# Optimization experiments

Hardware: AMD Instinct MI355X
Metric: run time of the kernel (lower is better)

Reference implementation:

```python
import jax, jax.numpy as jnp
import numpy as np

NUM_AGENTS = 256
STATE_DIM = 12 * NUM_AGENTS
CONTROL_DIM = 4 * NUM_AGENTS
MASS = 0.5
HIDDEN = 100
BATCH = 8192


def lambertw(x):
    # Principal branch for x >= 0 via Halley iterations (jit/vjp friendly).
    w = jnp.log1p(x)
    for _ in range(30):
        ew = jnp.exp(w)
        f = w * ew - x
        denom = ew * (w + 1.0) - (w + 2.0) * f / (2.0 * (w + 1.0))
        w = w - f / denom
    return w


def setup_inputs() -> dict:
    key = jax.random.key(0)
    ks = jax.random.split(key, 8)
    scale1 = 1.0 / np.sqrt(STATE_DIM + 1)
    scale2 = 1.0 / np.sqrt(HIDDEN)
    return {
        "z": jax.random.normal(ks[0], (BATCH, STATE_DIM), dtype=jnp.float32),
        "t": jax.random.uniform(ks[1], (BATCH, 1), dtype=jnp.float32),
        "W1": jax.random.normal(ks[2], (STATE_DIM + 1, HIDDEN), dtype=jnp.float32) * scale1,
        "b1": jnp.zeros((HIDDEN,), dtype=jnp.float32),
        "W2": jax.random.normal(ks[3], (HIDDEN, HIDDEN), dtype=jnp.float32) * scale2,
        "b2": jnp.zeros((HIDDEN,), dtype=jnp.float32),
        "W3": jax.random.normal(ks[4], (HIDDEN, STATE_DIM), dtype=jnp.float32) * scale2,
        "b3": jnp.zeros((STATE_DIM,), dtype=jnp.float32),
    }


def reference(z, t, W1, b1, W2, b2, W3, b3):
    # p_net: MLP on (t, z) producing cost parameters p (B, STATE_DIM)
    x = jnp.concatenate([t, z], axis=-1)
    h = jnp.tanh(x @ W1 + b1)
    h = jnp.tanh(h @ W2 + b2)
    p = h @ W3 + b3

    B = p.shape[0]
    pr = p.reshape(B, NUM_AGENTS, 12)
    # Linear cost vector c over controls: agent components (x,y,z adjoints)/m, psi, theta, phi.
    c = jnp.stack(
        [(pr[..., 6] + pr[..., 7] + pr[..., 8]) / MASS, pr[..., 9], pr[..., 10], pr[..., 11]],
        axis=-1,
    ).reshape(B, CONTROL_DIM)

    # Closed-form solution of min_u c^T u + exp(alpha * ||u||^2), alpha = 0.5/N:
    # u* = -k c with 2*alpha*k*exp(alpha*k^2*s) = 1, s = ||c||^2
    # => k = sqrt(W(s/(2*alpha)) / (2*alpha*s))
    alpha = 0.5 / NUM_AGENTS
    s = jnp.sum(c * c, axis=-1)  # (B,)
    w = lambertw(s / (2.0 * alpha))
    safe_s = jnp.where(s > 0, s, 1.0)
    k = jnp.sqrt(w / (2.0 * alpha * safe_s))
    k = jnp.where(s > 0, k, 0.0)
    ustar = -k[:, None] * c  # (B, CONTROL_DIM)
    return ustar
```

## Files before the change

### kernel.cpp

```cpp
#include <hip/hip_runtime.h>

#define DEV __device__ __forceinline__

typedef __bf16 bf16x8 __attribute__((ext_vector_type(8)));
typedef float f32x4 __attribute__((ext_vector_type(4)));
typedef short s16x8 __attribute__((ext_vector_type(8)));
typedef unsigned short u16x4 __attribute__((ext_vector_type(4)));
typedef unsigned short u16x8 __attribute__((ext_vector_type(8)));

constexpr int B_ = 8192;
constexpr int S_ = 3072;
constexpr int H_ = 100;
constexpr int NP_ = 128;
constexpr int C_ = 1024;
constexpr int KS_ = 64;
constexpr int NSPLIT_ = 4;
constexpr int KSP_ = S_ / NSPLIT_;
constexpr int NIT_ = KSP_ / KS_;

constexpr size_t OFF_W1b = 0;
constexpr size_t OFF_W2b = OFF_W1b + (size_t)NP_ * S_ * 2;
constexpr size_t OFF_W3c = OFF_W2b + (size_t)NP_ * NP_ * 2;
constexpr size_t OFF_b3c = OFF_W3c + (size_t)C_ * NP_ * 2;
constexpr size_t OFF_part = OFF_b3c + (size_t)C_ * 4;

DEV unsigned short f2bf(float f) {
  union { float f; unsigned u; } x; x.f = f;
  return (unsigned short)((x.u + 0x7FFFu + ((x.u >> 16) & 1u)) >> 16);
}

DEV float lambertw0(float x) {
  float w = log1pf(x);
#pragma unroll
  for (int i = 0; i < 10; ++i) {
    float ew = expf(w);
    float f = fmaf(w, ew, -x);
    float wp1 = w + 1.0f;
    float den = ew * wp1 - (w + 2.0f) * f / (2.0f * wp1);
    w = w - f / den;
  }
  return w;
}

DEV void gload16(const void* g, void* l) {
  __builtin_amdgcn_global_load_lds((const __attribute__((address_space(1))) unsigned int*)g,
                                   (__attribute__((address_space(3))) unsigned int*)l, 16, 0, 0);
}

__global__ void k0_prep(const float* __restrict__ W1, const float* __restrict__ W2,
                        const float* __restrict__ W3, const float* __restrict__ b3,
                        unsigned char* __restrict__ ws) {
  int idx = blockIdx.x * 256 + threadIdx.x;
  constexpr int R1 = NP_ * S_;
  constexpr int R2 = R1 + NP_ * NP_;
  constexpr int R3 = R2 + C_ * NP_;
  constexpr int R4 = R3 + C_;
  if (idx < R1) {
    int n = idx / S_, k = idx - n * S_;
    float v = (n < H_) ? W1[(size_t)(k + 1) * H_ + n] : 0.0f;
    ((unsigned short*)(ws + OFF_W1b))[idx] = f2bf(v);
  } else if (idx < R2) {
    int j = idx - R1;
    int n = j >> 7, k = j & 127;
    float v = (n < H_ && k < H_) ? W2[(size_t)k * H_ + n] : 0.0f;
    ((unsigned short*)(ws + OFF_W2b))[j] = f2bf(v);
  } else if (idx < R3) {
    int j = idx - R2;
    int n = j >> 7, k = j & 127;
    float v = 0.0f;
    if (k < H_) {
      int a = n >> 2, cmp = n & 3;
      const float* row = W3 + (size_t)k * S_ + a * 12;
      v = (cmp == 0) ? 2.0f * (row[6] + row[7] + row[8]) : row[8 + cmp];
    }
    ((unsigned short*)(ws + OFF_W3c))[j] = f2bf(v);
  } else if (idx < R4) {
    int n = idx - R3;
    int a = n >> 2, cmp = n & 3;
    const float* row = b3 + a * 12;
    float v = (cmp == 0) ? 2.0f * (row[6] + row[7] + row[8]) : row[8 + cmp];
    ((float*)(ws + OFF_b3c))[n] = v;
  }
}

__global__ __launch_bounds__(256, 4) void k1_gemm1(
    const float* __restrict__ z, const unsigned char* __restrict__ wsr,
    float* __restrict__ part) {
  __shared__ __align__(16) unsigned char lds[40 * 1024];
  unsigned char* ldsA = lds;
  unsigned char* ldsB = lds + 8192;

  const int tid = threadIdx.x;
  const int lane = tid & 63;
  const int w = tid >> 6;
  const int m = w & 1;
  const int q = w >> 1;
  const int bid = blockIdx.x;
  const int rt = bid >> 2;
  const int h = bid & 3;
  const int rowbase = rt * 32;
  const int k0 = h * KSP_;

  const unsigned short* W1b = (const unsigned short*)(wsr + OFF_W1b);

  const int arow0 = tid >> 4;
  const int acolf = (tid & 15) * 4;
  const float* zp = z + (size_t)(rowbase + arow0) * S_ + k0 + acolf;
  const int aswz = ((arow0 & 7) << 4);
  const int abyte0 = arow0 * 128 + (tid & 15) * 8;
  const int abyte1 = (arow0 + 16) * 128 + (tid & 15) * 8;

  const int w4 = w * 4;
  const unsigned short* bsrc = W1b + (size_t)(w4 * 8 + (lane >> 3)) * S_ + k0
                               + (((lane & 7) ^ (lane >> 3)) * 8);

  const int r0 = m * 16 + (lane & 15);
  const int kb0 = (lane >> 4) * 16;

  f32x4 acc[4];
#pragma unroll
  for (int e = 0; e < 4; ++e) acc[e] = f32x4{0.f, 0.f, 0.f, 0.f};

#define GLOAD_B(bufoff, kof) do {                                            \
    _Pragma("unroll")                                                        \
    for (int s = 0; s < 4; ++s)                                              \
      gload16(bsrc + (size_t)s * 8 * S_ + (kof),                             \
              ldsB + (bufoff) + (w4 + s) * 1024);                            \
  } while (0)

#define STAGE_A(dst, Z0, Z1) do {                                            \
    u16x4 a0; a0[0] = f2bf((Z0).x); a0[1] = f2bf((Z0).y);                    \
    a0[2] = f2bf((Z0).z); a0[3] = f2bf((Z0).w);                              \
    u16x4 a1; a1[0] = f2bf((Z1).x); a1[1] = f2bf((Z1).y);                    \
    a1[2] = f2bf((Z1).z); a1[3] = f2bf((Z1).w);                              \
    *(u16x4*)((dst) + (abyte0 ^ aswz)) = a0;                                 \
    *(u16x4*)((dst) + (abyte1 ^ aswz)) = a1;                                 \
  } while (0)

#define COMPUTE(Ac, Bc) do {                                                 \
    bf16x8 a0 = *(const bf16x8*)((Ac) + ((r0 * 128 + 0 + kb0) ^ ((r0 & 7) << 4)));   \
    bf16x8 a1 = *(const bf16x8*)((Ac) + ((r0 * 128 + 64 + kb0) ^ ((r0 & 7) << 4)));  \
    _Pragma("unroll")                                                        \
    for (int e = 0; e < 4; ++e) {                                            \
      int n = q * 64 + e * 16 + (lane & 15);                                 \
      bf16x8 bb0 = *(const bf16x8*)((Bc) + ((n * 128 + 0 + kb0) ^ ((n & 7) << 4)));  \
      bf16x8 bb1 = *(const bf16x8*)((Bc) + ((n * 128 + 64 + kb0) ^ ((n & 7) << 4))); \
      acc[e] = __builtin_amdgcn_mfma_f32_16x16x32_bf16(a0, bb0, acc[e], 0, 0, 0);    \
      acc[e] = __builtin_amdgcn_mfma_f32_16x16x32_bf16(a1, bb1, acc[e], 0, 0, 0);    \
    }                                                                        \
  } while (0)

  GLOAD_B(0, 0);
  {
    float4 z0 = *(const float4*)(zp);
    float4 z1 = *(const float4*)(zp + (size_t)16 * S_);
    STAGE_A(ldsA, z0, z1);
  }
  __syncthreads();

  for (int it = 0; it < NIT_; ++it) {
    const int cur = it & 1;
    const bool more = (it + 1 < NIT_);
    float4 z0, z1;
    if (more) {
      GLOAD_B((cur ^ 1) * 16384, (size_t)(it + 1) * KS_);
      z0 = *(const float4*)(zp + (it + 1) * KS_);
      z1 = *(const float4*)(zp + (size_t)16 * S_ + (it + 1) * KS_);
    }
    COMPUTE(ldsA + cur * 4096, ldsB + cur * 16384);
    if (more) STAGE_A(ldsA + (cur ^ 1) * 4096, z0, z1);
    __syncthreads();
  }
#undef GLOAD_B
#undef STAGE_A
#undef COMPUTE

  float* pout = part + (size_t)h * B_ * NP_;
#pragma unroll
  for (int e = 0; e < 4; ++e) {
    int col = q * 64 + e * 16 + (lane & 15);
#pragma unroll
    for (int i = 0; i < 4; ++i) {
      int r = m * 16 + ((lane >> 4) << 2) + i;
      pout[(size_t)(rowbase + r) * NP_ + col] = acc[e][i];
    }
  }
}

__global__ __launch_bounds__(512, 2) void k2_fused(
    const float* __restrict__ part, const float* __restrict__ t,
    const float* __restrict__ W1, const float* __restrict__ b1,
    const float* __restrict__ b2, const unsigned char* __restrict__ wsr,
    float* __restrict__ uo) {
  __shared__ __align__(16) unsigned char ldsA[8192];
  __shared__ __align__(16) unsigned char ldsB[2][32768];
  __shared__ float s_part[32][4];
  __shared__ float k_lds[32];

  const int tid = threadIdx.x;
  const int lane = tid & 63;
  const int w = tid >> 6;
  const int m = w & 1;
  const int q = w >> 1;
  const int rowbase = blockIdx.x * 32;

  const unsigned short* W2b = (const unsigned short*)(wsr + OFF_W2b);
  const unsigned short* W3cb = (const unsigned short*)(wsr + OFF_W3c);
  const float* b3c = (const float*)(wsr + OFF_b3c);

  {
    const int row = tid >> 4;
    const int col0 = (tid & 15) * 8;
    const float* p0 = part + (size_t)(rowbase + row) * NP_ + col0;
    f32x4 v[2];
#pragma unroll
    for (int p = 0; p < 2; ++p) {
      v[p] = *(const f32x4*)(p0 + p * 4);
#pragma unroll
      for (int hh = 1; hh < NSPLIT_; ++hh) {
        f32x4 u2 = *(const f32x4*)(p0 + (size_t)hh * B_ * NP_ + p * 4);
        v[p][0] += u2[0]; v[p][1] += u2[1]; v[p][2] += u2[2]; v[p][3] += u2[3];
      }
    }
    const float tv = t[rowbase + row];
    u16x8 o;
#pragma unroll
    for (int j = 0; j < 8; ++j) {
      int col = col0 + j;
      float b1c = (col < H_) ? b1[col] : 0.0f;
      float w1t = (col < H_) ? W1[col] : 0.0f;
      float pre = v[j >> 2][j & 3] + b1c + tv * w1t;
      o[j] = f2bf(tanhf(pre));
    }
    *(u16x8*)(ldsA + ((row * 256 + col0 * 2) ^ ((row & 7) << 4))) = o;
  }
#pragma unroll
  for (int s = 0; s < 4; ++s) {
    int p = s * 512 + tid;
    int n = p >> 4, k16 = p & 15;
    s16x8 v2 = *(const s16x8*)(W2b + n * 128 + k16 * 8);
    *(s16x8*)(ldsB[1] + ((n * 256 + k16 * 16) ^ ((n & 7) << 4))) = v2;
    s16x8 v3 = *(const s16x8*)(W3cb + (size_t)n * NP_ + k16 * 8);
    *(s16x8*)(ldsB[0] + ((n * 256 + k16 * 16) ^ ((n & 7) << 4))) = v3;
  }
  if (tid < 128) s_part[tid >> 2][tid & 3] = 0.0f;
  __syncthreads();

  const int r0 = m * 16 + (lane & 15);
  const int kb0 = (lane >> 4) * 16;

  f32x4 acc2[2];
  acc2[0] = f32x4{0.f, 0.f, 0.f, 0.f};
  acc2[1] = f32x4{0.f, 0.f, 0.f, 0.f};
#pragma unroll
  for (int ks = 0; ks < 4; ++ks) {
    bf16x8 a = *(const bf16x8*)(ldsA + ((r0 * 256 + ks * 64 + kb0) ^ ((r0 & 7) << 4)));
#pragma unroll
    for (int e = 0; e < 2; ++e) {
      int n = (q * 2 + e) * 16 + (lane & 15);
      bf16x8 b = *(const bf16x8*)(ldsB[1] + ((n * 256 + ks * 64 + kb0) ^ ((n & 7) << 4)));
      acc2[e] = __builtin_amdgcn_mfma_f32_16x16x32_bf16(a, b, acc2[e], 0, 0, 0);
    }
  }
  __syncthreads();
#pragma unroll
  for (int e = 0; e < 2; ++e) {
    int col = (q * 2 + e) * 16 + (lane & 15);
    float b2c = (col < H_) ? b2[col] : 0.0f;
#pragma unroll
    for (int i = 0; i < 4; ++i) {
      int r = m * 16 + ((lane >> 4) << 2) + i;
      float hh = tanhf(acc2[e][i] + b2c);
      *(unsigned short*)(ldsA + ((r * 256 + col * 2) ^ ((r & 7) << 4))) = f2bf(hh);
    }
  }
  __syncthreads();

  bf16x8 af[4];
#pragma unroll
  for (int ks = 0; ks < 4; ++ks)
    af[ks] = *(const bf16x8*)(ldsA + ((r0 * 256 + ks * 64 + kb0) ^ ((r0 & 7) << 4)));

  f32x4 fr[16];
#pragma unroll
  for (int i = 0; i < 16; ++i) fr[i] = f32x4{0.f, 0.f, 0.f, 0.f};

#pragma unroll 8
  for (int ch = 0; ch < 8; ++ch) {
    const int cur = ch & 1;
    const bool more = ch < 7;
    s16x8 st0, st1, st2, st3;
    if (more) {
      int base = (ch + 1) * 128;
      { int p = tid;            int n = p >> 4, k16 = p & 15; st0 = *(const s16x8*)(W3cb + (size_t)(base + n) * NP_ + k16 * 8); }
      { int p = 512 + tid;      int n = p >> 4, k16 = p & 15; st1 = *(const s16x8*)(W3cb + (size_t)(base + n) * NP_ + k16 * 8); }
      { int p = 1024 + tid;     int n = p >> 4, k16 = p & 15; st2 = *(const s16x8*)(W3cb + (size_t)(base + n) * NP_ + k16 * 8); }
      { int p = 1536 + tid;     int n = p >> 4, k16 = p & 15; st3 = *(const s16x8*)(W3cb + (size_t)(base + n) * NP_ + k16 * 8); }
    }
#pragma unroll
    for (int e = 0; e < 2; ++e) {
      int nloc = (q + 4 * e) * 16 + (lane & 15);
#pragma unroll
      for (int ks = 0; ks < 4; ++ks) {
        bf16x8 b = *(const bf16x8*)(ldsB[cur] + ((nloc * 256 + ks * 64 + kb0) ^ ((nloc & 7) << 4)));
        fr[ch * 2 + e] = __builtin_amdgcn_mfma_f32_16x16x32_bf16(af[ks], b, fr[ch * 2 + e], 0, 0, 0);
      }
    }
    if (more) {
      unsigned char* Bn = ldsB[cur ^ 1];
      { int p = tid;        int n = p >> 4, k16 = p & 15; *(s16x8*)(Bn + ((n * 256 + k16 * 16) ^ ((n & 7) << 4))) = st0; }
      { int p = 512 + tid;  int n = p >> 4, k16 = p & 15; *(s16x8*)(Bn + ((n * 256 + k16 * 16) ^ ((n & 7) << 4))) = st1; }
      { int p = 1024 + tid; int n = p >> 4, k16 = p & 15; *(s16x8*)(Bn + ((n * 256 + k16 * 16) ^ ((n & 7) << 4))) = st2; }
      { int p = 1536 + tid; int n = p >> 4, k16 = p & 15; *(s16x8*)(Bn + ((n * 256 + k16 * 16) ^ ((n & 7) << 4))) = st3; }
    }
    __syncthreads();
  }

#pragma unroll
  for (int fi = 0; fi < 16; ++fi) {
    int ch = fi >> 1, e = fi & 1;
    int col = (ch * 8 + q + 4 * e) * 16 + (lane & 15);
    float bc = b3c[col];
    fr[fi][0] += bc; fr[fi][1] += bc; fr[fi][2] += bc; fr[fi][3] += bc;
  }
#pragma unroll
  for (int i = 0; i < 4; ++i) {
    float v = 0.f;
#pragma unroll
    for (int fi = 0; fi < 16; ++fi) v += fr[fi][i] * fr[fi][i];
    v += __shfl_xor(v, 1);
    v += __shfl_xor(v, 2);
    v += __shfl_xor(v, 4);
    v += __shfl_xor(v, 8);
    if ((lane & 15) == 0) s_part[m * 16 + ((lane >> 4) << 2) + i][q] = v;
  }
  __syncthreads();
  if (tid < 32) {
    float s = s_part[tid][0] + s_part[tid][1] + s_part[tid][2] + s_part[tid][3];
    float kk = 0.0f;
    if (s > 0.0f) {
      float wv = lambertw0(s * 256.0f);
      kk = sqrtf(wv * 256.0f / s);
    }
    k_lds[tid] = kk;
  }
  __syncthreads();
#pragma unroll
  for (int fi = 0; fi < 16; ++fi) {
    int ch = fi >> 1, e = fi & 1;
    int col = (ch * 8 + q + 4 * e) * 16 + (lane & 15);
#pragma unroll
    for (int i = 0; i < 4; ++i) {
      int r = m * 16 + ((lane >> 4) << 2) + i;
      uo[(size_t)(rowbase + r) * C_ + col] = -k_lds[r] * fr[fi][i];
    }
  }
}

extern "C" void kernel_launch(void* const* d_in, const int* in_sizes, int n_in,
                              void* d_out, int out_size, void* d_ws, size_t ws_size,
                              hipStream_t stream) {
  const float* z  = (const float*)d_in[0];
  const float* t  = (const float*)d_in[1];
  const float* W1 = (const float*)d_in[2];
  const float* b1 = (const float*)d_in[3];
  const float* W2 = (const float*)d_in[4];
  const float* b2 = (const float*)d_in[5];
  const float* W3 = (const float*)d_in[6];
  const float* b3 = (const float*)d_in[7];
  float* out = (float*)d_out;
  unsigned char* ws = (unsigned char*)d_ws;
  float* part = (float*)(ws + OFF_part);

  constexpr int PREP_ELEMS = NP_ * S_ + NP_ * NP_ + C_ * NP_ + C_;
  k0_prep<<<(PREP_ELEMS + 255) / 256, 256, 0, stream>>>(W1, W2, W3, b3, ws);
  k1_gemm1<<<B_ / 32 * NSPLIT_, 256, 0, stream>>>(z, ws, part);
  k2_fused<<<B_ / 32, 512, 0, stream>>>(part, t, W1, b1, b2, ws, out);
}
```

Baseline: 51.52 us.

## Shrink gemm1 row tile to 16 and drop LDS double buffering for occupancy

The first GEMM kernel now processes 16 rows per block instead of 32, so twice as many blocks launch, and each wave computes two 16-column tiles instead of four. The LDS double buffer is replaced by a single buffer with two barriers per iteration, cutting LDS use from 40KB to about 18KB, and launch bounds are raised to 8 blocks per CU. The aim is more occupancy and parallelism to hide memory latency. In exchange, every W1 tile is reloaded twice as often, and global loads no longer overlap with compute inside a block.

```diff
diff --git a/kernel.cpp b/kernel.cpp
--- a/kernel.cpp
+++ b/kernel.cpp
@@ -17,6 +17,7 @@
 constexpr int NSPLIT_ = 4;
 constexpr int KSP_ = S_ / NSPLIT_;
 constexpr int NIT_ = KSP_ / KS_;
+constexpr int MT_ = 16;
 
 constexpr size_t OFF_W1b = 0;
 constexpr size_t OFF_W2b = OFF_W1b + (size_t)NP_ * S_ * 2;
@@ -83,93 +84,81 @@
   }
 }
 
-__global__ __launch_bounds__(256, 4) void k1_gemm1(
+__global__ __launch_bounds__(256, 8) void k1_gemm1(
     const float* __restrict__ z, const unsigned char* __restrict__ wsr,
     float* __restrict__ part) {
-  __shared__ __align__(16) unsigned char lds[40 * 1024];
-  unsigned char* ldsA = lds;
-  unsigned char* ldsB = lds + 8192;
+  __shared__ __align__(16) unsigned char ldsA[2048];
+  __shared__ __align__(16) unsigned char ldsB[16384];
 
   const int tid = threadIdx.x;
   const int lane = tid & 63;
   const int w = tid >> 6;
-  const int m = w & 1;
-  const int q = w >> 1;
   const int bid = blockIdx.x;
   const int rt = bid >> 2;
   const int h = bid & 3;
-  const int rowbase = rt * 32;
+  const int rowbase = rt * MT_;
   const int k0 = h * KSP_;
 
   const unsigned short* W1b = (const unsigned short*)(wsr + OFF_W1b);
 
-  const int arow0 = tid >> 4;
-  const int acolf = (tid & 15) * 4;
-  const float* zp = z + (size_t)(rowbase + arow0) * S_ + k0 + acolf;
-  const int aswz = ((arow0 & 7) << 4);
-  const int abyte0 = arow0 * 128 + (tid & 15) * 8;
-  const int abyte1 = (arow0 + 16) * 128 + (tid & 15) * 8;
+  const int arow = tid >> 4;
+  const float* zp = z + (size_t)(rowbase + arow) * S_ + k0 + (tid & 15) * 4;
+  const int aswz = ((arow & 7) << 4);
+  const int abyte = arow * 128 + (tid & 15) * 8;
 
   const int w4 = w * 4;
   const unsigned short* bsrc = W1b + (size_t)(w4 * 8 + (lane >> 3)) * S_ + k0
                                + (((lane & 7) ^ (lane >> 3)) * 8);
 
-  const int r0 = m * 16 + (lane & 15);
+  const int r0 = lane & 15;
   const int kb0 = (lane >> 4) * 16;
 
-  f32x4 acc[4];
-#pragma unroll
-  for (int e = 0; e < 4; ++e) acc[e] = f32x4{0.f, 0.f, 0.f, 0.f};
-
-#define GLOAD_B(bufoff, kof) do {                                            \
+  f32x4 acc[2];
+  acc[0] = f32x4{0.f, 0.f, 0.f, 0.f};
+  acc[1] = f32x4{0.f, 0.f, 0.f, 0.f};
+
+#define GLOAD_B(kof) do {                                                    \
     _Pragma("unroll")                                                        \
     for (int s = 0; s < 4; ++s)                                              \
       gload16(bsrc + (size_t)s * 8 * S_ + (kof),                             \
-              ldsB + (bufoff) + (w4 + s) * 1024);                            \
+              ldsB + (w4 + s) * 1024);                                       \
   } while (0)
 
-#define STAGE_A(dst, Z0, Z1) do {                                            \
+#define STAGE_A(Z0) do {                                                     \
     u16x4 a0; a0[0] = f2bf((Z0).x); a0[1] = f2bf((Z0).y);                    \
     a0[2] = f2bf((Z0).z); a0[3] = f2bf((Z0).w);                              \
-    u16x4 a1; a1[0] = f2bf((Z1).x); a1[1] = f2bf((Z1).y);                    \
-    a1[2] = f2bf((Z1).z); a1[3] = f2bf((Z1).w);                              \
-    *(u16x4*)((dst) + (abyte0 ^ aswz)) = a0;                                 \
-    *(u16x4*)((dst) + (abyte1 ^ aswz)) = a1;                                 \
+    *(u16x4*)(ldsA + (abyte ^ aswz)) = a0;                                   \
   } while (0)
 
-#define COMPUTE(Ac, Bc) do {                                                 \
-    bf16x8 a0 = *(const bf16x8*)((Ac) + ((r0 * 128 + 0 + kb0) ^ ((r0 & 7) << 4)));   \
-    bf16x8 a1 = *(const bf16x8*)((Ac) + ((r0 * 128 + 64 + kb0) ^ ((r0 & 7) << 4)));  \
+#define COMPUTE() do {                                                       \
+    bf16x8 a0 = *(const bf16x8*)(ldsA + ((r0 * 128 + 0 + kb0) ^ ((r0 & 7) << 4)));   \
+    bf16x8 a1 = *(const bf16x8*)(ldsA + ((r0 * 128 + 64 + kb0) ^ ((r0 & 7) << 4)));  \
     _Pragma("unroll")                                                        \
-    for (int e = 0; e < 4; ++e) {                                            \
-      int n = q * 64 + e * 16 + (lane & 15);                                 \
-      bf16x8 bb0 = *(const bf16x8*)((Bc) + ((n * 128 + 0 + kb0) ^ ((n & 7) << 4)));  \
-      bf16x8 bb1 = *(const bf16x8*)((Bc) + ((n * 128 + 64 + kb0) ^ ((n & 7) << 4))); \
+    for (int e = 0; e < 2; ++e) {                                            \
+      int n = w * 32 + e * 16 + (lane & 15);                                 \
+      bf16x8 bb0 = *(const bf16x8*)(ldsB + ((n * 128 + 0 + kb0) ^ ((n & 7) << 4)));  \
+      bf16x8 bb1 = *(const bf16x8*)(ldsB + ((n * 128 + 64 + kb0) ^ ((n & 7) << 4))); \
       acc[e] = __builtin_amdgcn_mfma_f32_16x16x32_bf16(a0, bb0, acc[e], 0, 0, 0);    \
       acc[e] = __builtin_amdgcn_mfma_f32_16x16x32_bf16(a1, bb1, acc[e], 0, 0, 0);    \
     }                                                                        \
   } while (0)
 
-  GLOAD_B(0, 0);
+  GLOAD_B(0);
   {
     float4 z0 = *(const float4*)(zp);
-    float4 z1 = *(const float4*)(zp + (size_t)16 * S_);
-    STAGE_A(ldsA, z0, z1);
+    STAGE_A(z0);
   }
   __syncthreads();
 
   for (int it = 0; it < NIT_; ++it) {
-    const int cur = it & 1;
-    const bool more = (it + 1 < NIT_);
-    float4 z0, z1;
-    if (more) {
-      GLOAD_B((cur ^ 1) * 16384, (size_t)(it + 1) * KS_);
-      z0 = *(const float4*)(zp + (it + 1) * KS_);
-      z1 = *(const float4*)(zp + (size_t)16 * S_ + (it + 1) * KS_);
-    }
-    COMPUTE(ldsA + cur * 4096, ldsB + cur * 16384);
-    if (more) STAGE_A(ldsA + (cur ^ 1) * 4096, z0, z1);
-    __syncthreads();
+    COMPUTE();
+    if (it + 1 < NIT_) {
+      __syncthreads();
+      GLOAD_B((size_t)(it + 1) * KS_);
+      float4 zn = *(const float4*)(zp + (it + 1) * KS_);
+      STAGE_A(zn);
+      __syncthreads();
+    }
   }
 #undef GLOAD_B
 #undef STAGE_A
@@ -177,11 +166,11 @@
 
   float* pout = part + (size_t)h * B_ * NP_;
 #pragma unroll
-  for (int e = 0; e < 4; ++e) {
-    int col = q * 64 + e * 16 + (lane & 15);
+  for (int e = 0; e < 2; ++e) {
+    int col = w * 32 + e * 16 + (lane & 15);
 #pragma unroll
     for (int i = 0; i < 4; ++i) {
-      int r = m * 16 + ((lane >> 4) << 2) + i;
+      int r = ((lane >> 4) << 2) + i;
       pout[(size_t)(rowbase + r) * NP_ + col] = acc[e][i];
     }
   }
@@ -374,6 +363,6 @@
 
   constexpr int PREP_ELEMS = NP_ * S_ + NP_ * NP_ + C_ * NP_ + C_;
   k0_prep<<<(PREP_ELEMS + 255) / 256, 256, 0, stream>>>(W1, W2, W3, b3, ws);
-  k1_gemm1<<<B_ / 32 * NSPLIT_, 256, 0, stream>>>(z, ws, part);
+  k1_gemm1<<<(B_ / MT_) * NSPLIT_, 256, 0, stream>>>(z, ws, part);
   k2_fused<<<B_ / 32, 512, 0, stream>>>(part, t, W1, b1, b2, ws, out);
 }
```

Result: slower. 57.41 us (+11.4%).
